# Performance work log

Measured on AMD Instinct MI355X. Metric: run time of the kernel, lower is better.

The kernel has to match this reference:

```python
import jax, jax.numpy as jnp
import numpy as np

B, N, H, OBS, A = 64, 64, 128, 128, 16
TAU = 0.5
BN = B * N
SQRT_H = float(np.sqrt(H))
_ar = np.arange(N)
# off-diagonal gather indices: row i lists all j != i in increasing order,
# matching torch's eye-mask boolean select in row-major order
IDX = jnp.asarray(np.stack([np.concatenate([_ar[:i], _ar[i + 1:]]) for i in range(N)]))  # [N, N-1]


def setup_inputs() -> dict:
    key = jax.random.key(0)
    ks = jax.random.split(key, 26)
    w = lambda k, s: jax.random.normal(k, s, jnp.float32) * 0.05
    return {
        "obs": jax.random.normal(ks[0], (BN, OBS), jnp.float32),
        "lstm_h": jax.random.normal(ks[1], (BN, 1, H), jnp.float32),
        "lstm_c": jax.random.normal(ks[2], (BN, 1, H), jnp.float32),
        "masks": jnp.ones((BN, 1), jnp.float32),
        "W_enc": w(ks[3], (H, OBS)), "b_enc": jnp.zeros((H,), jnp.float32),
        "lstm_Wih": w(ks[4], (4 * H, H)), "lstm_Whh": w(ks[5], (4 * H, H)),
        "lstm_bih": jnp.zeros((4 * H,), jnp.float32), "lstm_bhh": jnp.zeros((4 * H,), jnp.float32),
        "gru_Wih_f": w(ks[6], (3 * H, 2 * H)), "gru_Whh_f": w(ks[7], (3 * H, H)),
        "gru_bih_f": jnp.zeros((3 * H,), jnp.float32), "gru_bhh_f": jnp.zeros((3 * H,), jnp.float32),
        "gru_Wih_b": w(ks[8], (3 * H, 2 * H)), "gru_Whh_b": w(ks[9], (3 * H, H)),
        "gru_bih_b": jnp.zeros((3 * H,), jnp.float32), "gru_bhh_b": jnp.zeros((3 * H,), jnp.float32),
        "W_hard": w(ks[10], (2, 2 * H)), "b_hard": jnp.zeros((2,), jnp.float32),
        "Wq": w(ks[11], (H, H)), "Wk": w(ks[12], (H, H)),
        "W_act": w(ks[13], (A, 2 * H)), "b_act": jnp.zeros((A,), jnp.float32),
        # fixed Gumbel noise for the gumbel-softmax (makes reference deterministic)
        "gumbel": -jnp.log(-jnp.log(jax.random.uniform(ks[14], (BN, N - 1, 2), jnp.float32, 1e-6, 1.0 - 1e-6))),
    }


def _gru_scan(x_seq, Wih, Whh, bih, bhh):
    # x_seq: [T, BN2, 2H] -> outputs [T, BN2, H]
    def step(hst, x):
        gi = x @ Wih.T + bih
        gh = hst @ Whh.T + bhh
        gi_r, gi_z, gi_n = jnp.split(gi, 3, -1)
        gh_r, gh_z, gh_n = jnp.split(gh, 3, -1)
        r = jax.nn.sigmoid(gi_r + gh_r)
        z = jax.nn.sigmoid(gi_z + gh_z)
        n = jnp.tanh(gi_n + r * gh_n)
        hn = (1.0 - z) * n + z * hst
        return hn, hn
    h0 = jnp.zeros((x_seq.shape[1], Whh.shape[1]), x_seq.dtype)
    _, outs = jax.lax.scan(step, h0, x_seq)
    return outs


def _forward(obs, lstm_h, lstm_c, masks, W_enc, b_enc, lstm_Wih, lstm_Whh, lstm_bih,
             lstm_bhh, gru_Wih_f, gru_Whh_f, gru_bih_f, gru_bhh_f, gru_Wih_b, gru_Whh_b,
             gru_bih_b, gru_bhh_b, W_hard, b_hard, Wq, Wk, W_act, b_act, gumbel):
    # MLP encoder
    h = jax.nn.relu(obs @ W_enc.T + b_enc)                       # [BN, H]
    # single-step LSTM (recurrent_N = 1), mask resets states
    hprev = lstm_h[:, 0] * masks
    cprev = lstm_c[:, 0] * masks
    gates = h @ lstm_Wih.T + lstm_bih + hprev @ lstm_Whh.T + lstm_bhh
    i, f, g, o = jnp.split(gates, 4, -1)
    c_new = jax.nn.sigmoid(f) * cprev + jax.nn.sigmoid(i) * jnp.tanh(g)
    h = jax.nn.sigmoid(o) * jnp.tanh(c_new)                      # [BN, H]
    h_new, c_out = h[:, None, :], c_new[:, None, :]
    hb = h.reshape(B, N, H)
    h_others = hb[:, IDX]                                        # [B, N, N-1, H]
    h_self = jnp.broadcast_to(hb[:, :, None, :], (B, N, N - 1, H))
    h_pair = jnp.concatenate([h_self, h_others], -1).reshape(BN, N - 1, 2 * H)
    # bidirectional GRU over the N-1 "other agents" axis
    xs = jnp.swapaxes(h_pair, 0, 1)                              # [N-1, BN, 2H]
    out_f = _gru_scan(xs, gru_Wih_f, gru_Whh_f, gru_bih_f, gru_bhh_f)
    out_b = _gru_scan(xs[::-1], gru_Wih_b, gru_Whh_b, gru_bih_b, gru_bhh_b)[::-1]
    gru_out = jnp.swapaxes(jnp.concatenate([out_f, out_b], -1), 0, 1)  # [BN, N-1, 2H]
    # hard attention: gumbel-softmax (straight-through), keep channel 1
    logits = gru_out @ W_hard.T + b_hard                         # [BN, N-1, 2]
    y_soft = jax.nn.softmax((logits + gumbel) / TAU, axis=-1)
    y_hard = jax.nn.one_hot(jnp.argmax(y_soft, -1), 2, dtype=y_soft.dtype)
    y = jax.lax.stop_gradient(y_hard - y_soft) + y_soft
    hard_w = y[:, :, 1].reshape(B, N, N - 1, 1)
    # soft attention (manual scaled dot product over other agents)
    q = (h @ Wq.T).reshape(B, N, H)
    k = (h @ Wk.T).reshape(B, N, H)
    k_others = k[:, IDX]                                         # [B, N, N-1, H]
    soft_w = jax.nn.softmax(jnp.einsum('bnh,bnmh->bnm', q, k_others) / SQRT_H, axis=-1)
    x = jnp.sum(h_others * hard_w * soft_w[..., None], axis=2).reshape(BN, H)
    # action head (Discrete, deterministic=True -> argmax)
    act_logits = jnp.concatenate([h, x], -1) @ W_act.T + b_act   # [BN, A]
    logp = jax.nn.log_softmax(act_logits, -1)
    actions = jnp.argmax(act_logits, -1)
    alp = jnp.take_along_axis(logp, actions[:, None], axis=-1)   # [BN, 1]
    return actions[:, None], alp, h_new, c_out


def reference(obs, lstm_h, lstm_c, masks, W_enc, b_enc, lstm_Wih, lstm_Whh, lstm_bih,
              lstm_bhh, gru_Wih_f, gru_Whh_f, gru_bih_f, gru_bhh_f, gru_Wih_b, gru_Whh_b,
              gru_bih_b, gru_bhh_b, W_hard, b_hard, Wq, Wk, W_act, b_act, gumbel):
    return _forward(obs, lstm_h, lstm_c, masks, W_enc, b_enc, lstm_Wih, lstm_Whh,
                    lstm_bih, lstm_bhh, gru_Wih_f, gru_Whh_f, gru_bih_f, gru_bhh_f,
                    gru_Wih_b, gru_Whh_b, gru_bih_b, gru_bhh_b, W_hard, b_hard,
                    Wq, Wk, W_act, b_act, gumbel)
```

## Files before the change

### kernel.cpp

```cpp
#include <hip/hip_runtime.h>
#include <hip/hip_bf16.h>
#include <math.h>

#define BB   64
#define NN   64
#define HH   128
#define OBS_ 128
#define AA   16
#define BN_  4096
#define NM   63
#define G3   384
#define G4   512
#define UVS  1792
#define LDSW 136

typedef _Float16 f16x8 __attribute__((ext_vector_type(8)));
typedef float    f32x4 __attribute__((ext_vector_type(4)));

__device__ __forceinline__ float fsig(float x) {
    return __builtin_amdgcn_rcpf(1.0f + __builtin_amdgcn_exp2f(-1.4426950408889634f * x));
}
__device__ __forceinline__ float ftanh(float x) {
    return 1.0f - 2.0f * __builtin_amdgcn_rcpf(1.0f + __builtin_amdgcn_exp2f(2.8853900817779268f * x));
}

__device__ __forceinline__ unsigned short h2u(_Float16 h) {
    union { _Float16 f; unsigned short u; } cv; cv.f = h; return cv.u;
}

template<bool DUAL, bool RELU, bool RMASK>
__global__ __launch_bounds__(256)
void gemm_mfma(const float* __restrict__ A, int lda,
               const float* __restrict__ A2, int lda2,
               const float* __restrict__ rmask,
               const float* __restrict__ Bs0, const float* __restrict__ Bs1,
               const float* __restrict__ Bs2, const float* __restrict__ Bs3,
               const float* __restrict__ Bs4, const float* __restrict__ Bs5,
               const float* __restrict__ Bd, int ldb, int ldb2, int tilesPerSeg,
               const float* __restrict__ bias0, const float* __restrict__ bias2,
               float* __restrict__ C, int ldc)
{
    __shared__ __align__(16) unsigned short aHi[64][LDSW];
    __shared__ __align__(16) unsigned short aLo[64][LDSW];

    const int t = threadIdx.x;
    const int w = t >> 6, l = t & 63, li = l & 15, lg = l >> 4;
    const int bx = blockIdx.x, by = blockIdx.y;
    int seg, tIdx;
    if (bx < 4 * tilesPerSeg) { seg = bx / tilesPerSeg; tIdx = bx % tilesPerSeg; }
    else { const int r2 = bx - 4 * tilesPerSeg; seg = 4 + (r2 >> 1); tIdx = r2 & 1; }
    const int cts = tIdx * 64;
    const float* Bseg = seg == 0 ? Bs0 : seg == 1 ? Bs1 : seg == 2 ? Bs2
                       : seg == 3 ? Bs3 : seg == 4 ? Bs4 : Bs5;
    const float* biasSeg = seg == 0 ? bias0 : seg == 2 ? bias2 : nullptr;
    const int ldbs = (seg < 4) ? ldb : ldb2;
    const int row0 = by * 64;
    const int cl = w * 16 + li;

    f32x4 accA[4], accB[4];
    #pragma unroll
    for (int rt = 0; rt < 4; ++rt) {
        accA[rt] = (f32x4){0.f,0.f,0.f,0.f};
        accB[rt] = (f32x4){0.f,0.f,0.f,0.f};
    }

    const int npass = DUAL ? 2 : 1;
    for (int pass = 0; pass < npass; ++pass) {
        const float* Ap = pass ? A2 : A;
        const int ldap = pass ? lda2 : lda;
        __syncthreads();
        {
            const int ar = t >> 2, kof = (t & 3) * 32;
            const float* src = Ap + (size_t)(row0 + ar) * ldap + kof;
            float mk = 1.0f;
            if (RMASK && pass == 1) mk = rmask[row0 + ar];
            #pragma unroll
            for (int q = 0; q < 8; ++q) {
                float4 v = *(const float4*)(src + q * 4);
                if (RMASK && pass == 1) { v.x *= mk; v.y *= mk; v.z *= mk; v.w *= mk; }
                float vv[4] = {v.x, v.y, v.z, v.w};
                unsigned int hi01, hi23, lo01, lo23;
                {
                    _Float16 h0 = (_Float16)vv[0], h1 = (_Float16)vv[1];
                    _Float16 h2 = (_Float16)vv[2], h3 = (_Float16)vv[3];
                    _Float16 l0 = (_Float16)((vv[0] - (float)h0) * 1024.0f);
                    _Float16 l1 = (_Float16)((vv[1] - (float)h1) * 1024.0f);
                    _Float16 l2 = (_Float16)((vv[2] - (float)h2) * 1024.0f);
                    _Float16 l3 = (_Float16)((vv[3] - (float)h3) * 1024.0f);
                    hi01 = (unsigned int)h2u(h0) | ((unsigned int)h2u(h1) << 16);
                    hi23 = (unsigned int)h2u(h2) | ((unsigned int)h2u(h3) << 16);
                    lo01 = (unsigned int)h2u(l0) | ((unsigned int)h2u(l1) << 16);
                    lo23 = (unsigned int)h2u(l2) | ((unsigned int)h2u(l3) << 16);
                }
                *(uint2*)&aHi[ar][kof + q * 4] = make_uint2(hi01, hi23);
                *(uint2*)&aLo[ar][kof + q * 4] = make_uint2(lo01, lo23);
            }
        }
        const float* Bp = (DUAL && pass) ? Bd : Bseg;
        const int ldbp = (DUAL && pass) ? ldb : ldbs;
        f16x8 bhi[4], blo[4];
        #pragma unroll
        for (int kt = 0; kt < 4; ++kt) {
            const float* srcB = Bp + (size_t)(cts + cl) * ldbp + kt * 32 + lg * 8;
            #pragma unroll
            for (int j = 0; j < 8; ++j) {
                float wv = srcB[j];
                _Float16 hi = (_Float16)wv;
                _Float16 lo = (_Float16)((wv - (float)hi) * 1024.0f);
                bhi[kt][j] = hi;
                blo[kt][j] = lo;
            }
        }
        __syncthreads();
        #pragma unroll
        for (int kt = 0; kt < 4; ++kt) {
            const int koff = kt * 32 + lg * 8;
            #pragma unroll
            for (int rt = 0; rt < 4; ++rt) {
                f16x8 ah = *(const f16x8*)&aHi[rt * 16 + li][koff];
                f16x8 al = *(const f16x8*)&aLo[rt * 16 + li][koff];
                accA[rt] = __builtin_amdgcn_mfma_f32_16x16x32_f16(ah, bhi[kt], accA[rt], 0, 0, 0);
                accB[rt] = __builtin_amdgcn_mfma_f32_16x16x32_f16(al, bhi[kt], accB[rt], 0, 0, 0);
                accB[rt] = __builtin_amdgcn_mfma_f32_16x16x32_f16(ah, blo[kt], accB[rt], 0, 0, 0);
            }
        }
    }

    const float bv = biasSeg ? biasSeg[cts + cl] : 0.0f;
    const int gcol = bx * 64 + cl;
    #pragma unroll
    for (int rt = 0; rt < 4; ++rt)
        #pragma unroll
        for (int rg = 0; rg < 4; ++rg) {
            float x = fmaf(accB[rt][rg], 9.765625e-4f, accA[rt][rg]) + bv;
            if (RELU) x = fmaxf(x, 0.0f);
            const int r = row0 + rt * 16 + lg * 4 + rg;
            C[(size_t)r * ldc + gcol] = x;
        }
}

__global__ void lstm_pointwise(const float* __restrict__ gates,
                               const float* __restrict__ bih, const float* __restrict__ bhh,
                               const float* __restrict__ lstm_c, const float* __restrict__ masks,
                               float* __restrict__ h,
                               float* __restrict__ out_h, float* __restrict__ out_c)
{
    int idx = blockIdx.x * 256 + threadIdx.x;
    int r = idx >> 7, c = idx & 127;
    const float* g = gates + (size_t)r * G4;
    float gi = g[c]        + bih[c]        + bhh[c];
    float gf = g[128 + c]  + bih[128 + c]  + bhh[128 + c];
    float gg = g[256 + c]  + bih[256 + c]  + bhh[256 + c];
    float go = g[384 + c]  + bih[384 + c]  + bhh[384 + c];
    float cprev = lstm_c[idx] * masks[r];
    float cn = fsig(gf) * cprev + fsig(gi) * ftanh(gg);
    float hn = fsig(go) * ftanh(cn);
    h[idx] = hn;
    out_h[idx] = hn;
    out_c[idx] = cn;
}

__global__ __launch_bounds__(512, 2)
void gru_scan(const float* __restrict__ WhhF, const float* __restrict__ WhhB,
              const float* __restrict__ bhhF, const float* __restrict__ bhhB,
              const float* __restrict__ uvqk,
              const float* __restrict__ Whard,
              float* __restrict__ partF, float* __restrict__ partB)
{
    __shared__ __align__(16) unsigned short hHi[2][32][LDSW];
    __shared__ __align__(16) unsigned short hLo[2][32][LDSW];
    __shared__ float partLds[32][64][2];

    const int t = threadIdx.x;
    const int dir = blockIdx.x >> 7;
    const int blk = blockIdx.x & 127;
    const int r0 = blk * 32;
    const int bbx = r0 >> 6;
    const int n0 = r0 & 63;
    const int w  = t >> 6;
    const int l  = t & 63;
    const int li = l & 15;
    const int lg = l >> 4;
    const int cl = w * 16 + li;

    const float* Whh = dir ? WhhB : WhhF;
    const float* bhh = dir ? bhhB : bhhF;
    const float* U   = uvqk + dir * 768;
    const float* V   = uvqk + dir * 768 + 384;
    float* part      = dir ? partB : partF;

    f16x8 Bhi[3][4], Blo[3][4];
    #pragma unroll
    for (int g = 0; g < 3; ++g)
        #pragma unroll
        for (int kt = 0; kt < 4; ++kt) {
            const float* src = Whh + (size_t)(g * 128 + cl) * 128 + kt * 32 + lg * 8;
            #pragma unroll
            for (int j = 0; j < 8; ++j) {
                float wv = src[j];
                _Float16 hi = (_Float16)wv;
                _Float16 lo = (_Float16)((wv - (float)hi) * 1024.0f);
                Bhi[g][kt][j] = hi;
                Blo[g][kt][j] = lo;
            }
        }

    const bool pw = (w < 2);
    f16x8 Phi[4], Plo[4];
    if (pw) {
        #pragma unroll
        for (int kt = 0; kt < 4; ++kt) {
            #pragma unroll
            for (int j = 0; j < 8; ++j) {
                float wv = (li < 2) ? Whard[li * 256 + dir * 128 + kt * 32 + lg * 8 + j] : 0.0f;
                _Float16 hi = (_Float16)wv;
                _Float16 lo = (_Float16)((wv - (float)hi) * 1024.0f);
                Phi[kt][j] = hi;
                Plo[kt][j] = lo;
            }
        }
    }

    const float bh_r = bhh[cl];
    const float bh_z = bhh[128 + cl];
    const float bh_n = bhh[256 + cl];
    float u_r[8], u_z[8], u_n[8];
    #pragma unroll
    for (int rt = 0; rt < 2; ++rt)
        #pragma unroll
        for (int rg = 0; rg < 4; ++rg) {
            const int idx = rt * 4 + rg;
            const int R = r0 + rt * 16 + lg * 4 + rg;
            const float* Ur = U + (size_t)R * UVS;
            u_r[idx] = Ur[cl]       + bh_r;
            u_z[idx] = Ur[128 + cl] + bh_z;
            u_n[idx] = Ur[256 + cl] + bh_n;
        }

    const int vbase = bbx << 6;
    float v0r, v0z, v0n, v1r, v1z, v1n;
    {
        const int tt0 = dir ? (NM - 1) : 0;
        const float* Vr0 = V + (size_t)(vbase + tt0) * UVS;
        const float* Vr1 = V + (size_t)(vbase + tt0 + 1) * UVS;
        v0r = Vr0[cl]; v0z = Vr0[128 + cl]; v0n = Vr0[256 + cl];
        v1r = Vr1[cl]; v1z = Vr1[128 + cl]; v1n = Vr1[256 + cl];
    }

    for (int i = t; i < 2 * 32 * LDSW; i += 512) {
        (&hHi[0][0][0])[i] = 0;
        (&hLo[0][0][0])[i] = 0;
    }
    float hreg[8] = {0.f,0.f,0.f,0.f,0.f,0.f,0.f,0.f};

    int cur = 0;
    __syncthreads();

    for (int s = 0; s < NM; ++s) {
        const int tt = dir ? (NM - 1 - s) : s;
        const int nxt = cur ^ 1;

        float p0r, p0z, p0n, p1r, p1z, p1n;
        {
            const int sn = (s + 1 < NM) ? s + 1 : s;
            const int ttn = dir ? (NM - 1 - sn) : sn;
            const float* Vr0 = V + (size_t)(vbase + ttn) * UVS;
            const float* Vr1 = V + (size_t)(vbase + ttn + 1) * UVS;
            p0r = Vr0[cl]; p0z = Vr0[128 + cl]; p0n = Vr0[256 + cl];
            p1r = Vr1[cl]; p1z = Vr1[128 + cl]; p1n = Vr1[256 + cl];
        }

        f32x4 a0[3], b0[3], pA, pB;
        a0[0] = a0[1] = a0[2] = (f32x4){0.f,0.f,0.f,0.f};
        b0[0] = b0[1] = b0[2] = (f32x4){0.f,0.f,0.f,0.f};
        pA = pB = (f32x4){0.f,0.f,0.f,0.f};
        #pragma unroll
        for (int kt = 0; kt < 4; ++kt) {
            const int koff = kt * 32 + lg * 8;
            f16x8 Ah = *(const f16x8*)&hHi[cur][li][koff];
            f16x8 Al = *(const f16x8*)&hLo[cur][li][koff];
            #pragma unroll
            for (int g = 0; g < 3; ++g) {
                a0[g] = __builtin_amdgcn_mfma_f32_16x16x32_f16(Ah, Bhi[g][kt], a0[g], 0, 0, 0);
                b0[g] = __builtin_amdgcn_mfma_f32_16x16x32_f16(Al, Bhi[g][kt], b0[g], 0, 0, 0);
                b0[g] = __builtin_amdgcn_mfma_f32_16x16x32_f16(Ah, Blo[g][kt], b0[g], 0, 0, 0);
            }
            if (w == 0) {
                pA = __builtin_amdgcn_mfma_f32_16x16x32_f16(Ah, Phi[kt], pA, 0, 0, 0);
                pB = __builtin_amdgcn_mfma_f32_16x16x32_f16(Al, Phi[kt], pB, 0, 0, 0);
                pB = __builtin_amdgcn_mfma_f32_16x16x32_f16(Ah, Plo[kt], pB, 0, 0, 0);
            }
        }
        #pragma unroll
        for (int rg = 0; rg < 4; ++rg) {
            const int row = lg * 4 + rg;
            const bool up = (tt >= n0 + row);
            const float gr = fmaf(b0[0][rg], 9.765625e-4f, a0[0][rg]);
            const float gz = fmaf(b0[1][rg], 9.765625e-4f, a0[1][rg]);
            const float gn = fmaf(b0[2][rg], 9.765625e-4f, a0[2][rg]);
            const float rr  = fsig(u_r[rg] + (up ? v1r : v0r) + gr);
            const float zz  = fsig(u_z[rg] + (up ? v1z : v0z) + gz);
            const float nn2 = ftanh(u_n[rg] + (up ? v1n : v0n) + rr * gn);
            const float hn = fmaf(zz, hreg[rg] - nn2, nn2);
            hreg[rg] = hn;
            _Float16 hi = (_Float16)hn;
            _Float16 lo = (_Float16)((hn - (float)hi) * 1024.0f);
            hHi[nxt][row][cl] = h2u(hi);
            hLo[nxt][row][cl] = h2u(lo);
        }
        if (w == 0 && s > 0 && li < 2) {
            const int ttp = dir ? (tt + 1) : (tt - 1);
            #pragma unroll
            for (int rg = 0; rg < 4; ++rg)
                partLds[lg * 4 + rg][ttp][li] = pA[rg] + pB[rg] * 9.765625e-4f;
        }

        f32x4 a1[3], b1[3];
        a1[0] = a1[1] = a1[2] = (f32x4){0.f,0.f,0.f,0.f};
        b1[0] = b1[1] = b1[2] = (f32x4){0.f,0.f,0.f,0.f};
        f32x4 qA, qB;
        qA = qB = (f32x4){0.f,0.f,0.f,0.f};
        #pragma unroll
        for (int kt = 0; kt < 4; ++kt) {
            const int koff = kt * 32 + lg * 8;
            f16x8 Ah = *(const f16x8*)&hHi[cur][16 + li][koff];
            f16x8 Al = *(const f16x8*)&hLo[cur][16 + li][koff];
            #pragma unroll
            for (int g = 0; g < 3; ++g) {
                a1[g] = __builtin_amdgcn_mfma_f32_16x16x32_f16(Ah, Bhi[g][kt], a1[g], 0, 0, 0);
                b1[g] = __builtin_amdgcn_mfma_f32_16x16x32_f16(Al, Bhi[g][kt], b1[g], 0, 0, 0);
                b1[g] = __builtin_amdgcn_mfma_f32_16x16x32_f16(Ah, Blo[g][kt], b1[g], 0, 0, 0);
            }
            if (w == 1) {
                qA = __builtin_amdgcn_mfma_f32_16x16x32_f16(Ah, Phi[kt], qA, 0, 0, 0);
                qB = __builtin_amdgcn_mfma_f32_16x16x32_f16(Al, Phi[kt], qB, 0, 0, 0);
                qB = __builtin_amdgcn_mfma_f32_16x16x32_f16(Ah, Plo[kt], qB, 0, 0, 0);
            }
        }
        #pragma unroll
        for (int rg = 0; rg < 4; ++rg) {
            const int row = 16 + lg * 4 + rg;
            const int idx = 4 + rg;
            const bool up = (tt >= n0 + row);
            const float gr = fmaf(b1[0][rg], 9.765625e-4f, a1[0][rg]);
            const float gz = fmaf(b1[1][rg], 9.765625e-4f, a1[1][rg]);
            const float gn = fmaf(b1[2][rg], 9.765625e-4f, a1[2][rg]);
            const float rr  = fsig(u_r[idx] + (up ? v1r : v0r) + gr);
            const float zz  = fsig(u_z[idx] + (up ? v1z : v0z) + gz);
            const float nn2 = ftanh(u_n[idx] + (up ? v1n : v0n) + rr * gn);
            const float hn = fmaf(zz, hreg[idx] - nn2, nn2);
            hreg[idx] = hn;
            _Float16 hi = (_Float16)hn;
            _Float16 lo = (_Float16)((hn - (float)hi) * 1024.0f);
            hHi[nxt][row][cl] = h2u(hi);
            hLo[nxt][row][cl] = h2u(lo);
        }
        if (w == 1 && s > 0 && li < 2) {
            const int ttp = dir ? (tt + 1) : (tt - 1);
            #pragma unroll
            for (int rg = 0; rg < 4; ++rg)
                partLds[16 + lg * 4 + rg][ttp][li] = qA[rg] + qB[rg] * 9.765625e-4f;
        }

        v0r = p0r; v0z = p0z; v0n = p0n;
        v1r = p1r; v1z = p1z; v1n = p1n;
        cur = nxt;
        __syncthreads();
    }

    if (pw) {
        f32x4 qA = (f32x4){0.f,0.f,0.f,0.f}, qB = (f32x4){0.f,0.f,0.f,0.f};
        #pragma unroll
        for (int kt = 0; kt < 4; ++kt) {
            const int koff = kt * 32 + lg * 8;
            f16x8 Ah = *(const f16x8*)&hHi[cur][w * 16 + li][koff];
            f16x8 Al = *(const f16x8*)&hLo[cur][w * 16 + li][koff];
            qA = __builtin_amdgcn_mfma_f32_16x16x32_f16(Ah, Phi[kt], qA, 0, 0, 0);
            qB = __builtin_amdgcn_mfma_f32_16x16x32_f16(Al, Phi[kt], qB, 0, 0, 0);
            qB = __builtin_amdgcn_mfma_f32_16x16x32_f16(Ah, Plo[kt], qB, 0, 0, 0);
        }
        if (li < 2) {
            const int ttl = dir ? 0 : NM - 1;
            #pragma unroll
            for (int rg = 0; rg < 4; ++rg) {
                const int row = w * 16 + lg * 4 + rg;
                partLds[row][ttl][li] = qA[rg] + qB[rg] * 9.765625e-4f;
            }
        }
    }
    __syncthreads();

    {
        const int row = t >> 4;
        const int seg = t & 15;
        float* dst = part + (size_t)(r0 + row) * (NM * 2);
        #pragma unroll
        for (int k = 0; k < 4; ++k) {
            const int m = seg * 4 + k;
            if (m < NM) {
                float2 v = *(const float2*)&partLds[row][m][0];
                *(float2*)&dst[m * 2] = v;
            }
        }
    }
}

__global__ __launch_bounds__(128)
void attn_final(const float* __restrict__ h, const float* __restrict__ qk,
                const float* __restrict__ partF, const float* __restrict__ partB,
                const float* __restrict__ bhard, const float* __restrict__ gum,
                const float* __restrict__ Wact, const float* __restrict__ bact,
                float* __restrict__ out_act, float* __restrict__ out_alp)
{
    const int r = blockIdx.x;
    const int bbx = r >> 6, n = r & 63;
    const int t = threadIdx.x;
    __shared__ float qsh[HH], wsh[NM], shh[HH], shx[HH];
    if (t < HH) { qsh[t] = qk[(size_t)r * UVS + t]; shh[t] = h[(size_t)r * HH + t]; }
    __syncthreads();
    if (t < 64) {
        float sc = -INFINITY;
        float hardv = 0.0f;
        if (t < NM) {
            const int idxm = t + (t >= n ? 1 : 0);
            const float4* kr = (const float4*)(qk + (size_t)((bbx << 6) + idxm) * UVS + 128);
            float s = 0.0f;
            #pragma unroll
            for (int j4 = 0; j4 < 32; ++j4) {
                float4 kv = kr[j4];
                float4 qv = *(const float4*)&qsh[j4 * 4];
                s += kv.x * qv.x + kv.y * qv.y + kv.z * qv.z + kv.w * qv.w;
            }
            sc = s * 0.088388347648318447f;
            const float2 pf = *(const float2*)(partF + ((size_t)r * NM + t) * 2);
            const float2 pb = *(const float2*)(partB + ((size_t)r * NM + t) * 2);
            const float2 gv = *(const float2*)(gum + ((size_t)r * NM + t) * 2);
            const float l0 = pf.x + pb.x + bhard[0] + gv.x;
            const float l1 = pf.y + pb.y + bhard[1] + gv.y;
            hardv = (l1 > l0) ? 1.0f : 0.0f;
        }
        float mx = sc;
        #pragma unroll
        for (int d = 32; d; d >>= 1) mx = fmaxf(mx, __shfl_xor(mx, d, 64));
        const float e = (t < NM) ? expf(sc - mx) : 0.0f;
        float sum = e;
        #pragma unroll
        for (int d = 32; d; d >>= 1) sum += __shfl_xor(sum, d, 64);
        if (t < NM) wsh[t] = hardv * e / sum;
    }
    __syncthreads();
    {
        const int j = t;
        float x = 0.0f;
        for (int m = 0; m < NM; ++m) {
            const int idxm = m + (m >= n ? 1 : 0);
            x = fmaf(wsh[m], h[(size_t)((bbx << 6) + idxm) * HH + j], x);
        }
        shx[j] = x;
    }
    __syncthreads();
    if (t < 16) {
        const float* wa = Wact + (size_t)t * 256;
        float acc = bact[t];
        #pragma unroll
        for (int j4 = 0; j4 < 32; ++j4) {
            float4 w1 = *(const float4*)&wa[j4 * 4];
            float4 hv = *(const float4*)&shh[j4 * 4];
            float4 w2 = *(const float4*)&wa[128 + j4 * 4];
            float4 xv = *(const float4*)&shx[j4 * 4];
            acc += w1.x * hv.x + w1.y * hv.y + w1.z * hv.z + w1.w * hv.w
                 + w2.x * xv.x + w2.y * xv.y + w2.z * xv.z + w2.w * xv.w;
        }
        float mx = acc; int am = t;
        #pragma unroll
        for (int d = 8; d; d >>= 1) {
            const float om = __shfl_xor(mx, d, 16);
            const int   oa = __shfl_xor(am, d, 16);
            if (om > mx || (om == mx && oa < am)) { mx = om; am = oa; }
        }
        const float e = expf(acc - mx);
        float sum = e;
        #pragma unroll
        for (int d = 8; d; d >>= 1) sum += __shfl_xor(sum, d, 16);
        if (t == 0) {
            out_act[r] = (float)am;
            out_alp[r] = -logf(sum);
        }
    }
}

extern "C" void kernel_launch(void* const* d_in, const int* in_sizes, int n_in,
                              void* d_out, int out_size, void* d_ws, size_t ws_size,
                              hipStream_t stream)
{
    const float* obs    = (const float*)d_in[0];
    const float* lstm_h = (const float*)d_in[1];
    const float* lstm_c = (const float*)d_in[2];
    const float* masks  = (const float*)d_in[3];
    const float* W_enc  = (const float*)d_in[4];
    const float* b_enc  = (const float*)d_in[5];
    const float* lWih   = (const float*)d_in[6];
    const float* lWhh   = (const float*)d_in[7];
    const float* lbih   = (const float*)d_in[8];
    const float* lbhh   = (const float*)d_in[9];
    const float* gWihf  = (const float*)d_in[10];
    const float* gWhhf  = (const float*)d_in[11];
    const float* gbihf  = (const float*)d_in[12];
    const float* gbhhf  = (const float*)d_in[13];
    const float* gWihb  = (const float*)d_in[14];
    const float* gWhhb  = (const float*)d_in[15];
    const float* gbihb  = (const float*)d_in[16];
    const float* gbhhb  = (const float*)d_in[17];
    const float* Whard  = (const float*)d_in[18];
    const float* bhard  = (const float*)d_in[19];
    const float* Wq     = (const float*)d_in[20];
    const float* Wk     = (const float*)d_in[21];
    const float* Wact   = (const float*)d_in[22];
    const float* bact   = (const float*)d_in[23];
    const float* gum    = (const float*)d_in[24];

    float* W = (float*)d_ws;
    float* h     = W; W += (size_t)BN_ * HH;
    float* henc  = W; W += (size_t)BN_ * HH;
    float* gates = W; W += (size_t)BN_ * G4;
    float* uvqk  = W; W += (size_t)BN_ * UVS;
    float* partF = W; W += (size_t)BN_ * NM * 2;
    float* partB = W; W += (size_t)BN_ * NM * 2;

    float* out_f   = (float*)d_out;
    float* out_act = out_f;
    float* out_alp = out_act + BN_;
    float* out_h   = out_alp + BN_;
    float* out_c   = out_h + (size_t)BN_ * HH;

    gemm_mfma<false, true, false><<<dim3(2, BN_ / 64), 256, 0, stream>>>(
        obs, OBS_, nullptr, 0, nullptr,
        W_enc, nullptr, nullptr, nullptr, nullptr, nullptr, nullptr,
        OBS_, OBS_, 2, b_enc, nullptr, henc, HH);
    gemm_mfma<true, false, true><<<dim3(8, BN_ / 64), 256, 0, stream>>>(
        henc, HH, lstm_h, HH, masks,
        lWih, nullptr, nullptr, nullptr, nullptr, nullptr, lWhh,
        HH, HH, 8, nullptr, nullptr, gates, G4);
    lstm_pointwise<<<BN_ * HH / 256, 256, 0, stream>>>(gates, lbih, lbhh, lstm_c, masks,
                                                       h, out_h, out_c);
    gemm_mfma<false, false, false><<<dim3(28, BN_ / 64), 256, 0, stream>>>(
        h, HH, nullptr, 0, nullptr,
        gWihf, gWihf + HH, gWihb, gWihb + HH, Wq, Wk, nullptr,
        2 * HH, HH, 6, gbihf, gbihb, uvqk, UVS);
    gru_scan<<<256, 512, 0, stream>>>(gWhhf, gWhhb, gbhhf, gbhhb, uvqk,
                                      Whard, partF, partB);
    attn_final<<<BN_, 128, 0, stream>>>(h, uvqk + 1536, partF, partB, bhard, gum,
                                        Wact, bact, out_act, out_alp);
}
```

Measured before the change: 232.0 us.

## Halve rows per GRU scan block and double the grid to 512 blocks

Each gru_scan block now handles 16 sequence rows instead of 32, so the per-step recurrence does one MFMA tile group instead of two, and the grid doubles to 512 blocks. The launch bound is raised to 4 blocks per SM, and LDS buffers, register arrays, and the partial-output store pattern shrink to match. The aim is to shorten the serial per-step critical path and spread the work over more CUs on a latency-bound 63-step scan. In exchange, every block repeats the Whh weight loading and fp16 hi/lo splitting, so that setup work doubles, and the higher occupancy target may squeeze registers.

```diff
diff --git a/kernel.cpp b/kernel.cpp
--- a/kernel.cpp
+++ b/kernel.cpp
@@ -160,21 +160,21 @@
     out_c[idx] = cn;
 }
 
-__global__ __launch_bounds__(512, 2)
+__global__ __launch_bounds__(512, 4)
 void gru_scan(const float* __restrict__ WhhF, const float* __restrict__ WhhB,
               const float* __restrict__ bhhF, const float* __restrict__ bhhB,
               const float* __restrict__ uvqk,
               const float* __restrict__ Whard,
               float* __restrict__ partF, float* __restrict__ partB)
 {
-    __shared__ __align__(16) unsigned short hHi[2][32][LDSW];
-    __shared__ __align__(16) unsigned short hLo[2][32][LDSW];
-    __shared__ float partLds[32][64][2];
+    __shared__ __align__(16) unsigned short hHi[2][16][LDSW];
+    __shared__ __align__(16) unsigned short hLo[2][16][LDSW];
+    __shared__ float partLds[16][64][2];
 
     const int t = threadIdx.x;
-    const int dir = blockIdx.x >> 7;
-    const int blk = blockIdx.x & 127;
-    const int r0 = blk * 32;
+    const int dir = blockIdx.x >> 8;
+    const int blk = blockIdx.x & 255;
+    const int r0 = blk * 16;
     const int bbx = r0 >> 6;
     const int n0 = r0 & 63;
     const int w  = t >> 6;
@@ -205,9 +205,8 @@
             }
         }
 
-    const bool pw = (w < 2);
     f16x8 Phi[4], Plo[4];
-    if (pw) {
+    if (w == 0) {
         #pragma unroll
         for (int kt = 0; kt < 4; ++kt) {
             #pragma unroll
@@ -224,18 +223,15 @@
     const float bh_r = bhh[cl];
     const float bh_z = bhh[128 + cl];
     const float bh_n = bhh[256 + cl];
-    float u_r[8], u_z[8], u_n[8];
+    float u_r[4], u_z[4], u_n[4];
     #pragma unroll
-    for (int rt = 0; rt < 2; ++rt)
-        #pragma unroll
-        for (int rg = 0; rg < 4; ++rg) {
-            const int idx = rt * 4 + rg;
-            const int R = r0 + rt * 16 + lg * 4 + rg;
-            const float* Ur = U + (size_t)R * UVS;
-            u_r[idx] = Ur[cl]       + bh_r;
-            u_z[idx] = Ur[128 + cl] + bh_z;
-            u_n[idx] = Ur[256 + cl] + bh_n;
-        }
+    for (int rg = 0; rg < 4; ++rg) {
+        const int R = r0 + lg * 4 + rg;
+        const float* Ur = U + (size_t)R * UVS;
+        u_r[rg] = Ur[cl]       + bh_r;
+        u_z[rg] = Ur[128 + cl] + bh_z;
+        u_n[rg] = Ur[256 + cl] + bh_n;
+    }
 
     const int vbase = bbx << 6;
     float v0r, v0z, v0n, v1r, v1z, v1n;
@@ -247,11 +243,11 @@
         v1r = Vr1[cl]; v1z = Vr1[128 + cl]; v1n = Vr1[256 + cl];
     }
 
-    for (int i = t; i < 2 * 32 * LDSW; i += 512) {
+    for (int i = t; i < 2 * 16 * LDSW; i += 512) {
         (&hHi[0][0][0])[i] = 0;
         (&hLo[0][0][0])[i] = 0;
     }
-    float hreg[8] = {0.f,0.f,0.f,0.f,0.f,0.f,0.f,0.f};
+    float hreg[4] = {0.f,0.f,0.f,0.f};
 
     int cur = 0;
     __syncthreads();
@@ -291,6 +287,14 @@
                 pB = __builtin_amdgcn_mfma_f32_16x16x32_f16(Ah, Plo[kt], pB, 0, 0, 0);
             }
         }
+
+        if (w == 0 && s > 0 && li < 2) {
+            const int ttp = dir ? (tt + 1) : (tt - 1);
+            #pragma unroll
+            for (int rg = 0; rg < 4; ++rg)
+                partLds[lg * 4 + rg][ttp][li] = pA[rg] + pB[rg] * 9.765625e-4f;
+        }
+
         #pragma unroll
         for (int rg = 0; rg < 4; ++rg) {
             const int row = lg * 4 + rg;
@@ -308,59 +312,6 @@
             hHi[nxt][row][cl] = h2u(hi);
             hLo[nxt][row][cl] = h2u(lo);
         }
-        if (w == 0 && s > 0 && li < 2) {
-            const int ttp = dir ? (tt + 1) : (tt - 1);
-            #pragma unroll
-            for (int rg = 0; rg < 4; ++rg)
-                partLds[lg * 4 + rg][ttp][li] = pA[rg] + pB[rg] * 9.765625e-4f;
-        }
-
-        f32x4 a1[3], b1[3];
-        a1[0] = a1[1] = a1[2] = (f32x4){0.f,0.f,0.f,0.f};
-        b1[0] = b1[1] = b1[2] = (f32x4){0.f,0.f,0.f,0.f};
-        f32x4 qA, qB;
-        qA = qB = (f32x4){0.f,0.f,0.f,0.f};
-        #pragma unroll
-        for (int kt = 0; kt < 4; ++kt) {
-            const int koff = kt * 32 + lg * 8;
-            f16x8 Ah = *(const f16x8*)&hHi[cur][16 + li][koff];
-            f16x8 Al = *(const f16x8*)&hLo[cur][16 + li][koff];
-            #pragma unroll
-            for (int g = 0; g < 3; ++g) {
-                a1[g] = __builtin_amdgcn_mfma_f32_16x16x32_f16(Ah, Bhi[g][kt], a1[g], 0, 0, 0);
-                b1[g] = __builtin_amdgcn_mfma_f32_16x16x32_f16(Al, Bhi[g][kt], b1[g], 0, 0, 0);
-                b1[g] = __builtin_amdgcn_mfma_f32_16x16x32_f16(Ah, Blo[g][kt], b1[g], 0, 0, 0);
-            }
-            if (w == 1) {
-                qA = __builtin_amdgcn_mfma_f32_16x16x32_f16(Ah, Phi[kt], qA, 0, 0, 0);
-                qB = __builtin_amdgcn_mfma_f32_16x16x32_f16(Al, Phi[kt], qB, 0, 0, 0);
-                qB = __builtin_amdgcn_mfma_f32_16x16x32_f16(Ah, Plo[kt], qB, 0, 0, 0);
-            }
-        }
-        #pragma unroll
-        for (int rg = 0; rg < 4; ++rg) {
-            const int row = 16 + lg * 4 + rg;
-            const int idx = 4 + rg;
-            const bool up = (tt >= n0 + row);
-            const float gr = fmaf(b1[0][rg], 9.765625e-4f, a1[0][rg]);
-            const float gz = fmaf(b1[1][rg], 9.765625e-4f, a1[1][rg]);
-            const float gn = fmaf(b1[2][rg], 9.765625e-4f, a1[2][rg]);
-            const float rr  = fsig(u_r[idx] + (up ? v1r : v0r) + gr);
-            const float zz  = fsig(u_z[idx] + (up ? v1z : v0z) + gz);
-            const float nn2 = ftanh(u_n[idx] + (up ? v1n : v0n) + rr * gn);
-            const float hn = fmaf(zz, hreg[idx] - nn2, nn2);
-            hreg[idx] = hn;
-            _Float16 hi = (_Float16)hn;
-            _Float16 lo = (_Float16)((hn - (float)hi) * 1024.0f);
-            hHi[nxt][row][cl] = h2u(hi);
-            hLo[nxt][row][cl] = h2u(lo);
-        }
-        if (w == 1 && s > 0 && li < 2) {
-            const int ttp = dir ? (tt + 1) : (tt - 1);
-            #pragma unroll
-            for (int rg = 0; rg < 4; ++rg)
-                partLds[16 + lg * 4 + rg][ttp][li] = qA[rg] + qB[rg] * 9.765625e-4f;
-        }
 
         v0r = p0r; v0z = p0z; v0n = p0n;
         v1r = p1r; v1z = p1z; v1n = p1n;
@@ -368,13 +319,13 @@
         __syncthreads();
     }
 
-    if (pw) {
+    if (w == 0) {
         f32x4 qA = (f32x4){0.f,0.f,0.f,0.f}, qB = (f32x4){0.f,0.f,0.f,0.f};
         #pragma unroll
         for (int kt = 0; kt < 4; ++kt) {
             const int koff = kt * 32 + lg * 8;
-            f16x8 Ah = *(const f16x8*)&hHi[cur][w * 16 + li][koff];
-            f16x8 Al = *(const f16x8*)&hLo[cur][w * 16 + li][koff];
+            f16x8 Ah = *(const f16x8*)&hHi[cur][li][koff];
+            f16x8 Al = *(const f16x8*)&hLo[cur][li][koff];
             qA = __builtin_amdgcn_mfma_f32_16x16x32_f16(Ah, Phi[kt], qA, 0, 0, 0);
             qB = __builtin_amdgcn_mfma_f32_16x16x32_f16(Al, Phi[kt], qB, 0, 0, 0);
             qB = __builtin_amdgcn_mfma_f32_16x16x32_f16(Ah, Plo[kt], qB, 0, 0, 0);
@@ -382,21 +333,19 @@
         if (li < 2) {
             const int ttl = dir ? 0 : NM - 1;
             #pragma unroll
-            for (int rg = 0; rg < 4; ++rg) {
-                const int row = w * 16 + lg * 4 + rg;
-                partLds[row][ttl][li] = qA[rg] + qB[rg] * 9.765625e-4f;
-            }
+            for (int rg = 0; rg < 4; ++rg)
+                partLds[lg * 4 + rg][ttl][li] = qA[rg] + qB[rg] * 9.765625e-4f;
         }
     }
     __syncthreads();
 
     {
-        const int row = t >> 4;
-        const int seg = t & 15;
+        const int row = t >> 5;
+        const int seg = t & 31;
         float* dst = part + (size_t)(r0 + row) * (NM * 2);
         #pragma unroll
-        for (int k = 0; k < 4; ++k) {
-            const int m = seg * 4 + k;
+        for (int k = 0; k < 2; ++k) {
+            const int m = seg * 2 + k;
             if (m < NM) {
                 float2 v = *(const float2*)&partLds[row][m][0];
                 *(float2*)&dst[m * 2] = v;
@@ -547,7 +496,7 @@
         h, HH, nullptr, 0, nullptr,
         gWihf, gWihf + HH, gWihb, gWihb + HH, Wq, Wk, nullptr,
         2 * HH, HH, 6, gbihf, gbihb, uvqk, UVS);
-    gru_scan<<<256, 512, 0, stream>>>(gWhhf, gWhhb, gbhhf, gbhhb, uvqk,
+    gru_scan<<<512, 512, 0, stream>>>(gWhhf, gWhhb, gbhhf, gbhhb, uvqk,
                                       Whard, partF, partB);
     attn_final<<<BN_, 128, 0, stream>>>(h, uvqk + 1536, partF, partB, bhard, gum,
                                         Wact, bact, out_act, out_alp);
```

After: 772.6 us. 233% more time.
